# Performance work log

Measured on AMD Instinct MI355X. Metric: run time of the kernel, lower is better.

## Reference

```python
import jax, jax.numpy as jnp
import numpy as np

C = 256
C8 = C // 8

def setup_inputs() -> dict:
    key = jax.random.key(0)
    ks = jax.random.split(key, 7)
    B, H, W = 4, 64, 64
    x = jax.random.normal(ks[0], (B, C, H, W), dtype=jnp.float32)
    s = 1.0 / np.sqrt(C)
    Wq = jax.random.normal(ks[1], (C8, C), dtype=jnp.float32) * s
    bq = jnp.zeros((C8,), dtype=jnp.float32)
    Wk = jax.random.normal(ks[2], (C8, C), dtype=jnp.float32) * s
    bk = jnp.zeros((C8,), dtype=jnp.float32)
    Wv = jax.random.normal(ks[3], (C, C), dtype=jnp.float32) * s
    bv = jnp.zeros((C,), dtype=jnp.float32)
    return {"x": x, "Wq": Wq, "bq": bq, "Wk": Wk, "bk": bk, "Wv": Wv, "bv": bv}

def reference(x, Wq, bq, Wk, bk, Wv, bv):
    B, Cc, H, W = x.shape
    xf = x.reshape(B, Cc, H * W)                      # [B, C, N]
    # 1x1 convs == per-pixel linear projections
    q = jnp.einsum('dc,bcn->bdn', Wq, xf) + bq[None, :, None]   # [B, C/8, N]
    k = jnp.einsum('dc,bcn->bdn', Wk, xf) + bk[None, :, None]   # [B, C/8, N]
    v = jnp.einsum('dc,bcn->bdn', Wv, xf) + bv[None, :, None]   # [B, C,   N]
    scores = jnp.einsum('bdi,bdj->bij', q, k)         # [B, N, N] (no scaling, matching source)
    attn = jax.nn.softmax(scores, axis=-1)
    out = jnp.einsum('bcj,bij->bci', v, attn)         # [B, C, N]
    return out.reshape(B, Cc, H, W) + x
```

## Files before the change

kernel.cpp:

```cpp
#include <hip/hip_runtime.h>
#include <math.h>

#define CCH   256
#define NPIX  4096
#define BATCH 4

typedef __attribute__((ext_vector_type(8))) short    s16x8;
typedef __attribute__((ext_vector_type(4))) short    s16x4;
typedef __attribute__((ext_vector_type(8))) _Float16 f16x8;
typedef __attribute__((ext_vector_type(4))) float    f32x4;

__device__ __forceinline__ unsigned short f2bf(float f) {
    unsigned int u = __float_as_uint(f);
    u += 0x7fff + ((u >> 16) & 1);
    return (unsigned short)(u >> 16);
}
__device__ __forceinline__ float bf2f(unsigned short h) {
    return __uint_as_float(((unsigned int)h) << 16);
}
__device__ __forceinline__ unsigned short f2h(float f) {
    _Float16 h = (_Float16)f;
    return *(unsigned short*)&h;
}
__device__ __forceinline__ float h2f(unsigned short u) {
    _Float16 h = *(_Float16*)&u;
    return (float)h;
}

__device__ __forceinline__ size_t qk_addr(int b, int n, int d) {
    return ((((size_t)b * 256 + (n >> 4)) * 64 + ((d >> 3) << 4) + (n & 15)) << 3) + (d & 7);
}
__device__ __forceinline__ size_t v_addr(int b, int j, int c) {
    return ((((((size_t)b * 64 + (j >> 6)) * 16 + (c >> 4)) * 2 + ((j >> 5) & 1)) * 64
            + (((j >> 3) & 3) << 4) + (c & 15)) << 3) + (j & 7);
}

__global__ __launch_bounds__(64) void wcast_kernel(
    const float* __restrict__ Wq, const float* __restrict__ bq,
    const float* __restrict__ Wk, const float* __restrict__ bk,
    const float* __restrict__ Wv, const float* __restrict__ bv,
    unsigned short* __restrict__ wfh, unsigned short* __restrict__ wfl,
    float* __restrict__ bias_ws)
{
    const int rt = blockIdx.x;
    const int lane = threadIdx.x, l15 = lane & 15, quad = lane >> 4;
    const float *Ws, *bs; int roff; float scale = 1.0f;
    if (rt < 2)      { Ws = Wq; bs = bq; roff = rt * 16;      scale = 1.44269504f; }
    else if (rt < 4) { Ws = Wk; bs = bk; roff = (rt - 2) * 16; }
    else             { Ws = Wv; bs = bv; roff = (rt - 4) * 16; }

    const float* wrow = Ws + (size_t)(roff + l15) * CCH + quad * 8;
    for (int kb = 0; kb < 8; ++kb) {
        s16x8 h, l;
        #pragma unroll
        for (int d = 0; d < 8; ++d) {
            float wv = wrow[kb * 32 + d] * scale;
            unsigned short hh = f2h(wv);
            h[d] = (short)hh;
            l[d] = (short)f2h(wv - h2f(hh));
        }
        *(s16x8*)&wfh[(((size_t)rt * 8 + kb) * 64 + lane) * 8] = h;
        if (rt < 4) *(s16x8*)&wfl[(((size_t)rt * 8 + kb) * 64 + lane) * 8] = l;
    }
    if (lane < 16) bias_ws[rt * 16 + lane] = bs[roff + lane] * scale;
}

__global__ __launch_bounds__(256, 4) void proj_kernel(
    const float* __restrict__ x,
    const unsigned short* __restrict__ wfh, const unsigned short* __restrict__ wfl,
    const float* __restrict__ bias_ws,
    unsigned short* __restrict__ q_hi, unsigned short* __restrict__ k_hi,
    unsigned short* __restrict__ v_frag)
{
    const int t = threadIdx.x;
    const int rh = t >> 6, lane = t & 63, l15 = lane & 15, quad = lane >> 4;
    const int b = blockIdx.y;
    const int nt = blockIdx.x;

    const float* xb = x + (size_t)b * CCH * NPIX + nt * 16 + l15;

    f32x4 aq0 = {0.f, 0.f, 0.f, 0.f};
    f32x4 aq1 = {0.f, 0.f, 0.f, 0.f};
    f32x4 av[4];
    #pragma unroll
    for (int i = 0; i < 4; ++i) av[i] = (f32x4){0.f, 0.f, 0.f, 0.f};

    #pragma unroll 2
    for (int kb = 0; kb < 8; ++kb) {
        f16x8 xh, xl;
        #pragma unroll
        for (int d = 0; d < 8; ++d) {
            float xv = xb[(size_t)(kb * 32 + quad * 8 + d) * NPIX];
            _Float16 hh = (_Float16)xv;
            xh[d] = hh;
            xl[d] = (_Float16)(xv - (float)hh);
        }
        {
            const f16x8 ah = *(const f16x8*)&wfh[(((size_t)rh * 8 + kb) * 64 + lane) * 8];
            const f16x8 al = *(const f16x8*)&wfl[(((size_t)rh * 8 + kb) * 64 + lane) * 8];
            aq0 = __builtin_amdgcn_mfma_f32_16x16x32_f16(ah, xh, aq0, 0, 0, 0);
            aq1 = __builtin_amdgcn_mfma_f32_16x16x32_f16(ah, xl, aq1, 0, 0, 0);
            aq1 = __builtin_amdgcn_mfma_f32_16x16x32_f16(al, xh, aq1, 0, 0, 0);
        }
        #pragma unroll
        for (int i = 0; i < 4; ++i) {
            const int rt = 4 + rh * 4 + i;
            const f16x8 ah = *(const f16x8*)&wfh[(((size_t)rt * 8 + kb) * 64 + lane) * 8];
            av[i] = __builtin_amdgcn_mfma_f32_16x16x32_f16(ah, xh, av[i], 0, 0, 0);
        }
    }

    const int n = nt * 16 + l15;
    {
        s16x4 h4;
        #pragma unroll
        for (int rr = 0; rr < 4; ++rr) {
            const int rloc = quad * 4 + rr;
            const float val = aq0[rr] + aq1[rr] + bias_ws[rh * 16 + rloc];
            h4[rr] = (short)f2h(val);
        }
        if (rh < 2) {
            const size_t a = qk_addr(b, n, rh * 16 + quad * 4);
            *(s16x4*)&q_hi[a] = h4;
        } else {
            const size_t a = qk_addr(b, n, (rh - 2) * 16 + quad * 4);
            *(s16x4*)&k_hi[a] = h4;
        }
    }
    #pragma unroll
    for (int i = 0; i < 4; ++i) {
        const int vt = rh * 4 + i;
        #pragma unroll
        for (int rr = 0; rr < 4; ++rr) {
            const int rloc = quad * 4 + rr;
            const float val = av[i][rr] + bias_ws[(4 + vt) * 16 + rloc];
            v_frag[v_addr(b, n, vt * 16 + rloc)] = f2bf(val);
        }
    }
}

#define BARRIER_LGKM() do { \
    asm volatile("s_waitcnt lgkmcnt(0)" ::: "memory"); \
    __builtin_amdgcn_s_barrier(); \
    asm volatile("" ::: "memory"); \
} while (0)

#define QK_STEP(KF, BUFC) do { \
    f32x4 a0 = __builtin_amdgcn_mfma_f32_16x16x32_f16((KF), qf0, (f32x4){0.f,0.f,0.f,0.f}, 0, 0, 0); \
    f32x4 a1 = __builtin_amdgcn_mfma_f32_16x16x32_f16((KF), qf1, (f32x4){0.f,0.f,0.f,0.f}, 0, 0, 0); \
    unsigned int u0 = __float_as_uint(__builtin_exp2f(a0[0])) + 0x8000u; \
    unsigned int u1 = __float_as_uint(__builtin_exp2f(a0[1])) + 0x8000u; \
    unsigned int u2 = __float_as_uint(__builtin_exp2f(a0[2])) + 0x8000u; \
    unsigned int u3 = __float_as_uint(__builtin_exp2f(a0[3])) + 0x8000u; \
    uint2 pv; \
    pv.x = __builtin_amdgcn_perm(u1, u0, 0x07060302u); \
    pv.y = __builtin_amdgcn_perm(u3, u2, 0x07060302u); \
    *(uint2*)&p_lds[jh][BUFC][0 * 2 + pfrag_jj][(prow * 16 + l15) * 8 + pcol] = pv; \
    u0 = __float_as_uint(__builtin_exp2f(a1[0])) + 0x8000u; \
    u1 = __float_as_uint(__builtin_exp2f(a1[1])) + 0x8000u; \
    u2 = __float_as_uint(__builtin_exp2f(a1[2])) + 0x8000u; \
    u3 = __float_as_uint(__builtin_exp2f(a1[3])) + 0x8000u; \
    uint2 pw; \
    pw.x = __builtin_amdgcn_perm(u1, u0, 0x07060302u); \
    pw.y = __builtin_amdgcn_perm(u3, u2, 0x07060302u); \
    *(uint2*)&p_lds[jh][BUFC][1 * 2 + pfrag_jj][(prow * 16 + l15) * 8 + pcol] = pw; \
} while (0)

#define ATTN_BODY(T, BUFC, KU, KL, DO_QK) do { \
    const int jt = jh * 32 + (T); \
     \
    const s16x8 pf0 = *(const s16x8*)&p_lds[jh][BUFC][0][lane * 8]; \
    const s16x8 pf1 = *(const s16x8*)&p_lds[jh][BUFC][1][lane * 8]; \
    const s16x8 pf2 = *(const s16x8*)&p_lds[jh][BUFC][2][lane * 8]; \
    const s16x8 pf3 = *(const s16x8*)&p_lds[jh][BUFC][3][lane * 8]; \
     \
    const size_t vbase = (((size_t)jt * 16 + ch * 4) * 2) * 512; \
    const s16x8 v0 = *(const s16x8*)(vb + vbase); \
    const s16x8 v1 = *(const s16x8*)(vb + vbase + 512); \
    const s16x8 v2 = *(const s16x8*)(vb + vbase + 1024); \
    const s16x8 v3 = *(const s16x8*)(vb + vbase + 1536); \
    if (DO_QK) { QK_STEP(KU, (BUFC) ^ 1); } \
     \
    { \
        const int tpp = ((T) + 2 < 32) ? (T) + 2 : 0; \
        const size_t koff = (size_t)((jh * 32 + tpp) * 4 + ch) * 512; \
        KL = *(const f16x8*)(khb + koff); \
    } \
     \
    if (ch == 0) { \
        lacc = __builtin_amdgcn_mfma_f32_16x16x32_bf16(ones, pf0, lacc, 0, 0, 0); \
        lacc = __builtin_amdgcn_mfma_f32_16x16x32_bf16(ones, pf1, lacc, 0, 0, 0); \
    } else if (ch == 1) { \
        lacc = __builtin_amdgcn_mfma_f32_16x16x32_bf16(ones, pf2, lacc, 0, 0, 0); \
        lacc = __builtin_amdgcn_mfma_f32_16x16x32_bf16(ones, pf3, lacc, 0, 0, 0); \
    } \
    BARRIER_LGKM(); \
     \
    const s16x8 v4 = *(const s16x8*)(vb + vbase + 2048); \
    const s16x8 v5 = *(const s16x8*)(vb + vbase + 2560); \
    const s16x8 v6 = *(const s16x8*)(vb + vbase + 3072); \
    const s16x8 v7 = *(const s16x8*)(vb + vbase + 3584); \
    __builtin_amdgcn_s_setprio(1); \
    acc[0] = __builtin_amdgcn_mfma_f32_16x16x32_bf16(v0, pf0, acc[0], 0, 0, 0); \
    acc[0] = __builtin_amdgcn_mfma_f32_16x16x32_bf16(v1, pf1, acc[0], 0, 0, 0); \
    acc[1] = __builtin_amdgcn_mfma_f32_16x16x32_bf16(v0, pf2, acc[1], 0, 0, 0); \
    acc[1] = __builtin_amdgcn_mfma_f32_16x16x32_bf16(v1, pf3, acc[1], 0, 0, 0); \
    acc[2] = __builtin_amdgcn_mfma_f32_16x16x32_bf16(v2, pf0, acc[2], 0, 0, 0); \
    acc[2] = __builtin_amdgcn_mfma_f32_16x16x32_bf16(v3, pf1, acc[2], 0, 0, 0); \
    acc[3] = __builtin_amdgcn_mfma_f32_16x16x32_bf16(v2, pf2, acc[3], 0, 0, 0); \
    acc[3] = __builtin_amdgcn_mfma_f32_16x16x32_bf16(v3, pf3, acc[3], 0, 0, 0); \
    acc[4] = __builtin_amdgcn_mfma_f32_16x16x32_bf16(v4, pf0, acc[4], 0, 0, 0); \
    acc[4] = __builtin_amdgcn_mfma_f32_16x16x32_bf16(v5, pf1, acc[4], 0, 0, 0); \
    acc[5] = __builtin_amdgcn_mfma_f32_16x16x32_bf16(v4, pf2, acc[5], 0, 0, 0); \
    acc[5] = __builtin_amdgcn_mfma_f32_16x16x32_bf16(v5, pf3, acc[5], 0, 0, 0); \
    acc[6] = __builtin_amdgcn_mfma_f32_16x16x32_bf16(v6, pf0, acc[6], 0, 0, 0); \
    acc[6] = __builtin_amdgcn_mfma_f32_16x16x32_bf16(v7, pf1, acc[6], 0, 0, 0); \
    acc[7] = __builtin_amdgcn_mfma_f32_16x16x32_bf16(v6, pf2, acc[7], 0, 0, 0); \
    acc[7] = __builtin_amdgcn_mfma_f32_16x16x32_bf16(v7, pf3, acc[7], 0, 0, 0); \
    __builtin_amdgcn_s_setprio(0); \
} while (0)

__global__ __launch_bounds__(512, 4) void attn_kernel(
    const unsigned short* __restrict__ q_hi,
    const unsigned short* __restrict__ k_hi,
    const unsigned short* __restrict__ v_frag,
    const float* __restrict__ x, float* __restrict__ out)
{
    __shared__ unsigned short p_lds[2][2][4][512];
    __shared__ f32x4 comb[2][4][4][64];
    __shared__ float lds_l[2][2][16];

    const int t = threadIdx.x;
    const int w = t >> 6, lane = t & 63, l15 = lane & 15, quad = lane >> 4;
    const int jh = w >> 2, ch = w & 3;

    const int f = blockIdx.x;
    const int xcd = f & 7;
    const int b = xcd >> 1;
    const int ib = ((xcd & 1) << 6) + (f >> 3);

    f16x8 qf0, qf1;
    {
        const size_t qo0 = ((size_t)b * 256 + ib * 2 + 0) * 512 + (size_t)lane * 8;
        const size_t qo1 = ((size_t)b * 256 + ib * 2 + 1) * 512 + (size_t)lane * 8;
        qf0 = *(const f16x8*)(q_hi + qo0);
        qf1 = *(const f16x8*)(q_hi + qo1);
    }

    const s16x8 ones = { (short)0x3F80, (short)0x3F80, (short)0x3F80, (short)0x3F80,
                         (short)0x3F80, (short)0x3F80, (short)0x3F80, (short)0x3F80 };

    f32x4 acc[8];
    #pragma unroll
    for (int i = 0; i < 8; ++i) acc[i] = (f32x4){0.f, 0.f, 0.f, 0.f};
    f32x4 lacc = {0.f, 0.f, 0.f, 0.f};

    const unsigned short* khb = k_hi + (size_t)b * 131072 + (size_t)lane * 8;
    const unsigned short* vb  = v_frag + (size_t)b * 1048576 + (size_t)lane * 8;

    const int prow = ((ch & 1) << 1) + (quad >> 1);
    const int pcol = ((quad & 1) << 2);
    const int pfrag_jj = ch >> 1;

    f16x8 ka, kb;
    {
        const size_t k0 = (size_t)((jh * 32 + 0) * 4 + ch) * 512;
        ka = *(const f16x8*)(khb + k0);
    }
    QK_STEP(ka, 0);
    {
        const size_t k1 = (size_t)((jh * 32 + 1) * 4 + ch) * 512;
        ka = *(const f16x8*)(khb + k1);
    }
    BARRIER_LGKM();

    #pragma unroll 1
    for (int t2 = 0; t2 < 16; ++t2) {
        ATTN_BODY(2 * t2,     0, ka, kb, 1);
        ATTN_BODY(2 * t2 + 1, 1, kb, ka, (t2 < 15));
    }

    if (ch < 2 && lane < 16) lds_l[jh][ch][lane] = lacc[0];
    if (jh == 0) {
        #pragma unroll
        for (int ct = 0; ct < 4; ++ct)
            comb[0][ch][ct][lane] = acc[ct * 2 + 1];
    } else {
        #pragma unroll
        for (int ct = 0; ct < 4; ++ct)
            comb[1][ch][ct][lane] = acc[ct * 2 + 0];
    }
    __syncthreads();
    const float linv = 1.f / (lds_l[0][jh][l15] + lds_l[1][jh][l15]);
    const int ibase = (ib * 2 + jh) * 16 + l15;
    #pragma unroll
    for (int ct = 0; ct < 4; ++ct) {
        f32x4 a;
        if (jh == 0) a = acc[ct * 2 + 0];
        else         a = acc[ct * 2 + 1];
        a += comb[1 - jh][ch][ct][lane];
        #pragma unroll
        for (int rr = 0; rr < 4; ++rr) {
            const int c = ch * 64 + ct * 16 + quad * 4 + rr;
            const size_t idx = ((size_t)b * CCH + c) * NPIX + ibase;
            out[idx] = a[rr] * linv + x[idx];
        }
    }
}

extern "C" void kernel_launch(void* const* d_in, const int* in_sizes, int n_in,
                              void* d_out, int out_size, void* d_ws, size_t ws_size,
                              hipStream_t stream) {
    const float* x  = (const float*)d_in[0];
    const float* Wq = (const float*)d_in[1];
    const float* bq = (const float*)d_in[2];
    const float* Wk = (const float*)d_in[3];
    const float* bk = (const float*)d_in[4];
    const float* Wv = (const float*)d_in[5];
    const float* bv = (const float*)d_in[6];
    float* out = (float*)d_out;

    unsigned short* ws = (unsigned short*)d_ws;
    unsigned short* q_hi   = ws;
    unsigned short* k_hi   = ws + 1048576;
    unsigned short* v_frag = ws + 2097152;
    unsigned short* wfh    = ws + 6291456;
    unsigned short* wfl    = ws + 6373376;
    float*          bias_ws = (float*)(ws + 6389760);

    wcast_kernel<<<20, 64, 0, stream>>>(Wq, bq, Wk, bk, Wv, bv, wfh, wfl, bias_ws);
    proj_kernel<<<dim3(256, BATCH), 256, 0, stream>>>(x, wfh, wfl, bias_ws,
                                                      q_hi, k_hi, v_frag);
    attn_kernel<<<512, 512, 0, stream>>>(q_hi, k_hi, v_frag, x, out);
}
```

Measured before the change: 145.0 us.

## Process two key tiles per barrier window in attention pipeline

Restructures the attention main loop so each barrier-separated window handles two key tiles instead of one. The P buffer in LDS doubles to four slots, and K prefetch distance grows to four and five tiles ahead. This halves the number of workgroup barriers and gives each window a longer MFMA run. The cost is more VGPRs for the extra V and P fragments, which under launch bounds of 512 threads with 4 blocks may cause spills or lower occupancy.

```diff
diff --git a/kernel.cpp b/kernel.cpp
--- a/kernel.cpp
+++ b/kernel.cpp
@@ -166,57 +166,73 @@
     *(uint2*)&p_lds[jh][BUFC][1 * 2 + pfrag_jj][(prow * 16 + l15) * 8 + pcol] = pw; \
 } while (0)
 
-#define ATTN_BODY(T, BUFC, KU, KL, DO_QK) do { \
-    const int jt = jh * 32 + (T); \
+#define PV8(VA, VB, PA, PB, PC, PD, I0, I1) do { \
+    acc[I0] = __builtin_amdgcn_mfma_f32_16x16x32_bf16((VA), (PA), acc[I0], 0, 0, 0); \
+    acc[I0] = __builtin_amdgcn_mfma_f32_16x16x32_bf16((VB), (PB), acc[I0], 0, 0, 0); \
+    acc[I1] = __builtin_amdgcn_mfma_f32_16x16x32_bf16((VA), (PC), acc[I1], 0, 0, 0); \
+    acc[I1] = __builtin_amdgcn_mfma_f32_16x16x32_bf16((VB), (PD), acc[I1], 0, 0, 0); \
+} while (0)
+
+#define ATTN_WIN(T, BR0, BR1, BW0, BW1, KU0, KU1, KL0, KL1, DO_QK) do { \
+    const int jtA = jh * 32 + (T); \
      \
-    const s16x8 pf0 = *(const s16x8*)&p_lds[jh][BUFC][0][lane * 8]; \
-    const s16x8 pf1 = *(const s16x8*)&p_lds[jh][BUFC][1][lane * 8]; \
-    const s16x8 pf2 = *(const s16x8*)&p_lds[jh][BUFC][2][lane * 8]; \
-    const s16x8 pf3 = *(const s16x8*)&p_lds[jh][BUFC][3][lane * 8]; \
+    const s16x8 pfA0 = *(const s16x8*)&p_lds[jh][BR0][0][lane * 8]; \
+    const s16x8 pfA1 = *(const s16x8*)&p_lds[jh][BR0][1][lane * 8]; \
+    const s16x8 pfA2 = *(const s16x8*)&p_lds[jh][BR0][2][lane * 8]; \
+    const s16x8 pfA3 = *(const s16x8*)&p_lds[jh][BR0][3][lane * 8]; \
+    const s16x8 pfB0 = *(const s16x8*)&p_lds[jh][BR1][0][lane * 8]; \
+    const s16x8 pfB1 = *(const s16x8*)&p_lds[jh][BR1][1][lane * 8]; \
+    const s16x8 pfB2 = *(const s16x8*)&p_lds[jh][BR1][2][lane * 8]; \
+    const s16x8 pfB3 = *(const s16x8*)&p_lds[jh][BR1][3][lane * 8]; \
+    const size_t vbaseA = (((size_t)jtA * 16 + ch * 4) * 2) * 512; \
+    const size_t vbaseB = vbaseA + 16384;   \
      \
-    const size_t vbase = (((size_t)jt * 16 + ch * 4) * 2) * 512; \
-    const s16x8 v0 = *(const s16x8*)(vb + vbase); \
-    const s16x8 v1 = *(const s16x8*)(vb + vbase + 512); \
-    const s16x8 v2 = *(const s16x8*)(vb + vbase + 1024); \
-    const s16x8 v3 = *(const s16x8*)(vb + vbase + 1536); \
-    if (DO_QK) { QK_STEP(KU, (BUFC) ^ 1); } \
-     \
+    const s16x8 vA0 = *(const s16x8*)(vb + vbaseA); \
+    const s16x8 vA1 = *(const s16x8*)(vb + vbaseA + 512); \
+    const s16x8 vA2 = *(const s16x8*)(vb + vbaseA + 1024); \
+    const s16x8 vA3 = *(const s16x8*)(vb + vbaseA + 1536); \
+    if (DO_QK) { QK_STEP(KU0, BW0); QK_STEP(KU1, BW1); } \
     { \
-        const int tpp = ((T) + 2 < 32) ? (T) + 2 : 0; \
-        const size_t koff = (size_t)((jh * 32 + tpp) * 4 + ch) * 512; \
-        KL = *(const f16x8*)(khb + koff); \
+        const int tp0 = ((T) + 4 < 32) ? (T) + 4 : 0; \
+        const int tp1 = ((T) + 5 < 32) ? (T) + 5 : 0; \
+        KL0 = *(const f16x8*)(khb + (size_t)((jh * 32 + tp0) * 4 + ch) * 512); \
+        KL1 = *(const f16x8*)(khb + (size_t)((jh * 32 + tp1) * 4 + ch) * 512); \
     } \
      \
     if (ch == 0) { \
-        lacc = __builtin_amdgcn_mfma_f32_16x16x32_bf16(ones, pf0, lacc, 0, 0, 0); \
-        lacc = __builtin_amdgcn_mfma_f32_16x16x32_bf16(ones, pf1, lacc, 0, 0, 0); \
+        lacc = __builtin_amdgcn_mfma_f32_16x16x32_bf16(ones, pfA0, lacc, 0, 0, 0); \
+        lacc = __builtin_amdgcn_mfma_f32_16x16x32_bf16(ones, pfA1, lacc, 0, 0, 0); \
+        lacc = __builtin_amdgcn_mfma_f32_16x16x32_bf16(ones, pfB0, lacc, 0, 0, 0); \
+        lacc = __builtin_amdgcn_mfma_f32_16x16x32_bf16(ones, pfB1, lacc, 0, 0, 0); \
     } else if (ch == 1) { \
-        lacc = __builtin_amdgcn_mfma_f32_16x16x32_bf16(ones, pf2, lacc, 0, 0, 0); \
-        lacc = __builtin_amdgcn_mfma_f32_16x16x32_bf16(ones, pf3, lacc, 0, 0, 0); \
+        lacc = __builtin_amdgcn_mfma_f32_16x16x32_bf16(ones, pfA2, lacc, 0, 0, 0); \
+        lacc = __builtin_amdgcn_mfma_f32_16x16x32_bf16(ones, pfA3, lacc, 0, 0, 0); \
+        lacc = __builtin_amdgcn_mfma_f32_16x16x32_bf16(ones, pfB2, lacc, 0, 0, 0); \
+        lacc = __builtin_amdgcn_mfma_f32_16x16x32_bf16(ones, pfB3, lacc, 0, 0, 0); \
     } \
     BARRIER_LGKM(); \
      \
-    const s16x8 v4 = *(const s16x8*)(vb + vbase + 2048); \
-    const s16x8 v5 = *(const s16x8*)(vb + vbase + 2560); \
-    const s16x8 v6 = *(const s16x8*)(vb + vbase + 3072); \
-    const s16x8 v7 = *(const s16x8*)(vb + vbase + 3584); \
+    const s16x8 vA4 = *(const s16x8*)(vb + vbaseA + 2048); \
+    const s16x8 vA5 = *(const s16x8*)(vb + vbaseA + 2560); \
+    const s16x8 vA6 = *(const s16x8*)(vb + vbaseA + 3072); \
+    const s16x8 vA7 = *(const s16x8*)(vb + vbaseA + 3584); \
+    const s16x8 vB0 = *(const s16x8*)(vb + vbaseB); \
+    const s16x8 vB1 = *(const s16x8*)(vb + vbaseB + 512); \
+    const s16x8 vB2 = *(const s16x8*)(vb + vbaseB + 1024); \
+    const s16x8 vB3 = *(const s16x8*)(vb + vbaseB + 1536); \
+    const s16x8 vB4 = *(const s16x8*)(vb + vbaseB + 2048); \
+    const s16x8 vB5 = *(const s16x8*)(vb + vbaseB + 2560); \
+    const s16x8 vB6 = *(const s16x8*)(vb + vbaseB + 3072); \
+    const s16x8 vB7 = *(const s16x8*)(vb + vbaseB + 3584); \
     __builtin_amdgcn_s_setprio(1); \
-    acc[0] = __builtin_amdgcn_mfma_f32_16x16x32_bf16(v0, pf0, acc[0], 0, 0, 0); \
-    acc[0] = __builtin_amdgcn_mfma_f32_16x16x32_bf16(v1, pf1, acc[0], 0, 0, 0); \
-    acc[1] = __builtin_amdgcn_mfma_f32_16x16x32_bf16(v0, pf2, acc[1], 0, 0, 0); \
-    acc[1] = __builtin_amdgcn_mfma_f32_16x16x32_bf16(v1, pf3, acc[1], 0, 0, 0); \
-    acc[2] = __builtin_amdgcn_mfma_f32_16x16x32_bf16(v2, pf0, acc[2], 0, 0, 0); \
-    acc[2] = __builtin_amdgcn_mfma_f32_16x16x32_bf16(v3, pf1, acc[2], 0, 0, 0); \
-    acc[3] = __builtin_amdgcn_mfma_f32_16x16x32_bf16(v2, pf2, acc[3], 0, 0, 0); \
-    acc[3] = __builtin_amdgcn_mfma_f32_16x16x32_bf16(v3, pf3, acc[3], 0, 0, 0); \
-    acc[4] = __builtin_amdgcn_mfma_f32_16x16x32_bf16(v4, pf0, acc[4], 0, 0, 0); \
-    acc[4] = __builtin_amdgcn_mfma_f32_16x16x32_bf16(v5, pf1, acc[4], 0, 0, 0); \
-    acc[5] = __builtin_amdgcn_mfma_f32_16x16x32_bf16(v4, pf2, acc[5], 0, 0, 0); \
-    acc[5] = __builtin_amdgcn_mfma_f32_16x16x32_bf16(v5, pf3, acc[5], 0, 0, 0); \
-    acc[6] = __builtin_amdgcn_mfma_f32_16x16x32_bf16(v6, pf0, acc[6], 0, 0, 0); \
-    acc[6] = __builtin_amdgcn_mfma_f32_16x16x32_bf16(v7, pf1, acc[6], 0, 0, 0); \
-    acc[7] = __builtin_amdgcn_mfma_f32_16x16x32_bf16(v6, pf2, acc[7], 0, 0, 0); \
-    acc[7] = __builtin_amdgcn_mfma_f32_16x16x32_bf16(v7, pf3, acc[7], 0, 0, 0); \
+    PV8(vA0, vA1, pfA0, pfA1, pfA2, pfA3, 0, 1); \
+    PV8(vA2, vA3, pfA0, pfA1, pfA2, pfA3, 2, 3); \
+    PV8(vA4, vA5, pfA0, pfA1, pfA2, pfA3, 4, 5); \
+    PV8(vA6, vA7, pfA0, pfA1, pfA2, pfA3, 6, 7); \
+    PV8(vB0, vB1, pfB0, pfB1, pfB2, pfB3, 0, 1); \
+    PV8(vB2, vB3, pfB0, pfB1, pfB2, pfB3, 2, 3); \
+    PV8(vB4, vB5, pfB0, pfB1, pfB2, pfB3, 4, 5); \
+    PV8(vB6, vB7, pfB0, pfB1, pfB2, pfB3, 6, 7); \
     __builtin_amdgcn_s_setprio(0); \
 } while (0)
 
@@ -226,7 +242,7 @@
     const unsigned short* __restrict__ v_frag,
     const float* __restrict__ x, float* __restrict__ out)
 {
-    __shared__ unsigned short p_lds[2][2][4][512];
+    __shared__ unsigned short p_lds[2][4][4][512];
     __shared__ f32x4 comb[2][4][4][64];
     __shared__ float lds_l[2][2][16];
 
@@ -262,22 +278,19 @@
     const int pcol = ((quad & 1) << 2);
     const int pfrag_jj = ch >> 1;
 
-    f16x8 ka, kb;
-    {
-        const size_t k0 = (size_t)((jh * 32 + 0) * 4 + ch) * 512;
-        ka = *(const f16x8*)(khb + k0);
-    }
+    f16x8 ka, kb, kc, kd;
+    ka = *(const f16x8*)(khb + (size_t)((jh * 32 + 0) * 4 + ch) * 512);
+    kb = *(const f16x8*)(khb + (size_t)((jh * 32 + 1) * 4 + ch) * 512);
     QK_STEP(ka, 0);
-    {
-        const size_t k1 = (size_t)((jh * 32 + 1) * 4 + ch) * 512;
-        ka = *(const f16x8*)(khb + k1);
-    }
+    QK_STEP(kb, 1);
+    ka = *(const f16x8*)(khb + (size_t)((jh * 32 + 2) * 4 + ch) * 512);
+    kb = *(const f16x8*)(khb + (size_t)((jh * 32 + 3) * 4 + ch) * 512);
     BARRIER_LGKM();
 
     #pragma unroll 1
-    for (int t2 = 0; t2 < 16; ++t2) {
-        ATTN_BODY(2 * t2,     0, ka, kb, 1);
-        ATTN_BODY(2 * t2 + 1, 1, kb, ka, (t2 < 15));
+    for (int w2 = 0; w2 < 8; ++w2) {
+        ATTN_WIN(4 * w2,     0, 1, 2, 3, ka, kb, kc, kd, 1);
+        ATTN_WIN(4 * w2 + 2, 2, 3, 0, 1, kc, kd, ka, kb, (w2 < 7));
     }
 
     if (ch < 2 && lane < 16) lds_l[jh][ch][lane] = lacc[0];
```

After: 256.9 us. +77.2%, slower.
